# Kernel optimization log

Measured on AMD Instinct MI355X. Metric: run time of the kernel, lower is better.

## Reference

```python
import math
import jax, jax.numpy as jnp
import numpy as np

DIM = 4096
N_HEADS = 32
N_KV_HEADS = 8
HEAD_DIM = DIM // N_HEADS  # 128
N_REP = N_HEADS // N_KV_HEADS  # 4
BSZ = 1
SEQLEN = 2048
ROPE_THETA = 500000.0


def setup_inputs() -> dict:
    key = jax.random.key(0)
    ks = jax.random.split(key, 8)
    s = 1.0 / math.sqrt(DIM)
    x = jax.random.normal(ks[0], (BSZ, SEQLEN, DIM), dtype=jnp.float32)
    wq = jax.random.normal(ks[1], (DIM, N_HEADS * HEAD_DIM), dtype=jnp.float32) * s
    wk = jax.random.normal(ks[2], (DIM, N_KV_HEADS * HEAD_DIM), dtype=jnp.float32) * s
    wv = jax.random.normal(ks[3], (DIM, N_KV_HEADS * HEAD_DIM), dtype=jnp.float32) * s
    wo = jax.random.normal(ks[4], (N_HEADS * HEAD_DIM, DIM), dtype=jnp.float32) * s
    # RoPE frequencies: freqs_cis[t, j] = exp(i * t * theta^{-2j/hd})
    inv_freq = 1.0 / (ROPE_THETA ** (jnp.arange(0, HEAD_DIM, 2, dtype=jnp.float32) / HEAD_DIM))
    t = jnp.arange(SEQLEN, dtype=jnp.float32)
    angles = jnp.outer(t, inv_freq)  # [S, hd/2]
    freqs_cos = jnp.cos(angles)
    freqs_sin = jnp.sin(angles)
    # causal additive mask [S, S]: 0 on/below diagonal, -inf above
    mask = jnp.triu(jnp.full((SEQLEN, SEQLEN), float('-inf'), dtype=jnp.float32), k=1)
    cache_k = jnp.zeros((BSZ, SEQLEN, N_KV_HEADS, HEAD_DIM), dtype=jnp.float32)
    cache_v = jnp.zeros((BSZ, SEQLEN, N_KV_HEADS, HEAD_DIM), dtype=jnp.float32)
    return {"x": x, "wq": wq, "wk": wk, "wv": wv, "wo": wo,
            "freqs_cos": freqs_cos, "freqs_sin": freqs_sin, "mask": mask,
            "cache_k": cache_k, "cache_v": cache_v, "start_pos": 0}


def _apply_rotary(xq, xk, cos, sin):
    # xq: [B,S,Hq,hd], xk: [B,S,Hkv,hd]; cos/sin: [S, hd/2]
    def rot(x):
        b, s, h, d = x.shape
        xr = x.reshape(b, s, h, d // 2, 2)
        a, bb = xr[..., 0], xr[..., 1]
        c = cos[None, :, None, :]
        sn = sin[None, :, None, :]
        out = jnp.stack([a * c - bb * sn, a * sn + bb * c], axis=-1)
        return out.reshape(b, s, h, d)
    return rot(xq), rot(xk)


def reference(x, wq, wk, wv, wo, freqs_cos, freqs_sin, mask, cache_k, cache_v, start_pos):
    bsz, seqlen, _ = x.shape
    xq = (x @ wq).reshape(bsz, seqlen, N_HEADS, HEAD_DIM)
    xk = (x @ wk).reshape(bsz, seqlen, N_KV_HEADS, HEAD_DIM)
    xv = (x @ wv).reshape(bsz, seqlen, N_KV_HEADS, HEAD_DIM)
    xq, xk = _apply_rotary(xq, xk, freqs_cos, freqs_sin)
    # KV-cache append
    cache_k = jax.lax.dynamic_update_slice(cache_k, xk, (0, start_pos, 0, 0))
    cache_v = jax.lax.dynamic_update_slice(cache_v, xv, (0, start_pos, 0, 0))
    kv_len = start_pos + seqlen
    keys = cache_k[:, :kv_len]    # [B, T, Hkv, hd]
    values = cache_v[:, :kv_len]
    # GQA repeat (logical; einsum reshaping keeps math identical)
    keys = jnp.repeat(keys, N_REP, axis=2)      # [B, T, Hq, hd]
    values = jnp.repeat(values, N_REP, axis=2)
    scale = 1.0 / math.sqrt(HEAD_DIM)
    scores = jnp.einsum('bqhd,bkhd->bhqk', xq, keys) * scale
    scores = scores + mask[None, None, :, :kv_len]
    probs = jax.nn.softmax(scores.astype(jnp.float32), axis=-1).astype(xq.dtype)
    out = jnp.einsum('bhqk,bkhd->bqhd', probs, values)
    out = out.reshape(bsz, seqlen, N_HEADS * HEAD_DIM)
    return out @ wo
```

## Files before the change

### kernel.cpp

```cpp
#include <hip/hip_runtime.h>
#include <hip/hip_bf16.h>

typedef unsigned short u16;
typedef short short8 __attribute__((ext_vector_type(8)));
typedef float floatx4 __attribute__((ext_vector_type(4)));

#define DIM 4096
#define SEQ 2048
#define NH 32
#define NKV 8
#define HD 128
#define QKV_N 6144

static __device__ __forceinline__ float b2f(u16 u) {
    return __uint_as_float(((unsigned int)u) << 16);
}
static __device__ __forceinline__ u16 f2b(float f) {
    unsigned int u = __float_as_uint(f);
    u = (u + 0x7FFFu + ((u >> 16) & 1u)) >> 16;
    return (u16)u;
}
static __device__ __forceinline__ void async16(const u16* g, u16* l) {
    __builtin_amdgcn_global_load_lds((const __attribute__((address_space(1))) void*)g,
                                     (__attribute__((address_space(3))) void*)l, 16, 0, 0);
}

__global__ __launch_bounds__(256) void transpose_f32_bf16(const float* __restrict__ src,
                                                          u16* __restrict__ dst,
                                                          int R, int C) {
    __shared__ u16 tile[32][33];
    int c0 = blockIdx.x * 32, r0 = blockIdx.y * 32;
    int x = threadIdx.x & 31, y0 = threadIdx.x >> 5;
#pragma unroll
    for (int i = 0; i < 4; i++) {
        int r = y0 + i * 8;
        tile[r][x] = f2b(src[(size_t)(r0 + r) * C + c0 + x]);
    }
    __syncthreads();
#pragma unroll
    for (int i = 0; i < 4; i++) {
        int r = y0 + i * 8;
        dst[(size_t)(c0 + r) * R + r0 + x] = tile[x][r];
    }
}

__global__ __launch_bounds__(256) void convert_f32_bf16(const float* __restrict__ src,
                                                        u16* __restrict__ dst) {
    int i = (blockIdx.x * 256 + threadIdx.x) * 4;
    float4 f = *(const float4*)(src + i);
    ushort4 o;
    o.x = f2b(f.x); o.y = f2b(f.y); o.z = f2b(f.z); o.w = f2b(f.w);
    *(ushort4*)(dst + i) = o;
}

__global__ __launch_bounds__(256) void transpose_v(const u16* __restrict__ Xqkv,
                                                   u16* __restrict__ VT) {
    __shared__ u16 tile[32][33];
    int k0 = blockIdx.x * 32, d0 = blockIdx.y * 32, h = blockIdx.z;
    const u16* src = Xqkv + DIM + NKV * HD + h * HD;
    int x = threadIdx.x & 31, y0 = threadIdx.x >> 5;
#pragma unroll
    for (int i = 0; i < 4; i++) {
        int r = y0 + i * 8;
        tile[r][x] = src[(size_t)(k0 + r) * QKV_N + d0 + x];
    }
    __syncthreads();
    u16* dst = VT + ((size_t)h * HD + d0) * SEQ + k0;
#pragma unroll
    for (int i = 0; i < 4; i++) {
        int r = y0 + i * 8;
        dst[(size_t)r * SEQ + x] = tile[x][r];
    }
}

template<bool CF32>
__global__ __launch_bounds__(256) void gemm_bf16(const u16* __restrict__ A,
                                                 const u16* __restrict__ Bt,
                                                 void* __restrict__ Cv,
                                                 int M, int N, int K) {
    __shared__ u16 As[128 * 32];
    __shared__ u16 Bs[128 * 32];
    int tid = threadIdx.x;
    int wave = tid >> 6, lane = tid & 63, quad = lane >> 4, l16 = lane & 15;
    int wrow = (wave >> 1) * 64, wcol = (wave & 1) * 64;
    int m0 = blockIdx.y * 128, n0 = blockIdx.x * 128;

    int g = (lane & 3) ^ ((lane >> 3) & 3);
    int srow = lane >> 2;
    const u16* Ap = A + (size_t)(m0 + wave * 32 + srow) * K + g * 8;
    const u16* Bp = Bt + (size_t)(n0 + wave * 32 + srow) * K + g * 8;
    u16* As0 = &As[wave * 1024];
    u16* Bs0 = &Bs[wave * 1024];
    int sA = quad ^ ((l16 >> 1) & 3);

    floatx4 acc[4][4];
#pragma unroll
    for (int i = 0; i < 4; i++)
#pragma unroll
        for (int j = 0; j < 4; j++) acc[i][j] = (floatx4){0.f, 0.f, 0.f, 0.f};

    int nk = K >> 5;
    for (int kb = 0; kb < nk; kb++) {
        __syncthreads();
        const u16* a0 = Ap + kb * 32;
        const u16* b0 = Bp + kb * 32;
        async16(a0, As0);
        async16(a0 + (size_t)16 * K, As0 + 512);
        async16(b0, Bs0);
        async16(b0 + (size_t)16 * K, Bs0 + 512);
        __syncthreads();
        short8 a[4], b[4];
#pragma unroll
        for (int mt = 0; mt < 4; mt++)
            a[mt] = *(const short8*)&As[(wrow + mt * 16 + l16) * 32 + sA * 8];
#pragma unroll
        for (int nt = 0; nt < 4; nt++)
            b[nt] = *(const short8*)&Bs[(wcol + nt * 16 + l16) * 32 + sA * 8];
#pragma unroll
        for (int mt = 0; mt < 4; mt++)
#pragma unroll
            for (int nt = 0; nt < 4; nt++)
                acc[mt][nt] = __builtin_amdgcn_mfma_f32_16x16x32_bf16(a[mt], b[nt], acc[mt][nt], 0, 0, 0);
    }

#pragma unroll
    for (int mt = 0; mt < 4; mt++)
#pragma unroll
        for (int nt = 0; nt < 4; nt++) {
            int row = m0 + wrow + mt * 16 + quad * 4;
            int col = n0 + wcol + nt * 16 + l16;
#pragma unroll
            for (int r = 0; r < 4; r++) {
                if constexpr (CF32)
                    ((float*)Cv)[(size_t)(row + r) * N + col] = acc[mt][nt][r];
                else
                    ((u16*)Cv)[(size_t)(row + r) * N + col] = f2b(acc[mt][nt][r]);
            }
        }
}

__global__ __launch_bounds__(256) void rope_kernel(u16* __restrict__ X,
                                                   const float* __restrict__ fc,
                                                   const float* __restrict__ fs) {
    int idx = blockIdx.x * 256 + threadIdx.x;
    int i = idx & 63;
    int rem = idx >> 6;
    int h = rem % 40;
    int pos = rem / 40;
    int col = (h < 32) ? (h * 128 + 2 * i) : (4096 + (h - 32) * 128 + 2 * i);
    size_t off = (size_t)pos * QKV_N + col;
    unsigned int pr = *(unsigned int*)&X[off];
    float a = b2f((u16)(pr & 0xffffu));
    float b = b2f((u16)(pr >> 16));
    float c = fc[pos * 64 + i];
    float s = fs[pos * 64 + i];
    float na = a * c - b * s;
    float nb = a * s + b * c;
    unsigned int outw = ((unsigned int)f2b(nb) << 16) | (unsigned int)f2b(na);
    *(unsigned int*)&X[off] = outw;
}

__global__ __launch_bounds__(256) void attn_kernel(const u16* __restrict__ Xqkv,
                                                   const u16* __restrict__ VT,
                                                   u16* __restrict__ O) {
    __shared__ u16 Ks[64 * 128];
    __shared__ u16 Vt[128 * 64];
    __shared__ u16 Ps[4 * 1024];
    int head = blockIdx.y;
    int kvh = head >> 2;
    const u16* Xq = Xqkv + head * HD;
    const u16* Xk = Xqkv + DIM + kvh * HD;
    const u16* Vg = VT + (size_t)kvh * HD * SEQ;
    int tid = threadIdx.x, wave = tid >> 6, lane = tid & 63, quad = lane >> 4, l16 = lane & 15;

    size_t offKe = (size_t)quad * QKV_N + (size_t)((l16 ^ quad) * 8);
    size_t offKo = (size_t)quad * QKV_N + (size_t)((l16 ^ (quad + 4)) * 8);
    size_t offV  = (size_t)(lane >> 3) * SEQ + (size_t)((((lane & 7) ^ ((lane >> 3) & 7))) * 8);
    int sK[4];
#pragma unroll
    for (int ks = 0; ks < 4; ks++) sK[ks] = (ks * 4 + quad) ^ (l16 & 7);

    const float scale = 0.08838834764831845f;

    for (int pass = 0; pass < 2; pass++) {
        int qb = pass ? (31 - blockIdx.x) : blockIdx.x;
        int q0 = qb * 64;

        short8 aq[4];
        {
            const u16* qp = Xq + (size_t)(q0 + wave * 16 + l16) * QKV_N + quad * 8;
#pragma unroll
            for (int ks = 0; ks < 4; ks++) aq[ks] = *(const short8*)(qp + ks * 32);
        }
        float l_i[4] = {0.f, 0.f, 0.f, 0.f};
        floatx4 o_acc[8];
#pragma unroll
        for (int i = 0; i < 8; i++) o_acc[i] = (floatx4){0.f, 0.f, 0.f, 0.f};

        for (int kb = 0; kb <= qb; kb++) {
            __syncthreads();
#pragma unroll
            for (int c = 0; c < 4; c++) {
                int kc = wave * 4 + c;
                const u16* gp = Xk + (size_t)(kb * 64 + kc * 4) * QKV_N + ((kc & 1) ? offKo : offKe);
                async16(gp, &Ks[kc * 512]);
            }
#pragma unroll
            for (int c = 0; c < 4; c++) {
                int vc = wave * 4 + c;
                async16(Vg + (size_t)(vc * 8) * SEQ + (size_t)(kb * 64) + offV, &Vt[vc * 512]);
            }
            __syncthreads();

            floatx4 s[4];
#pragma unroll
            for (int nt = 0; nt < 4; nt++) s[nt] = (floatx4){0.f, 0.f, 0.f, 0.f};
#pragma unroll
            for (int ks = 0; ks < 4; ks++) {
#pragma unroll
                for (int nt = 0; nt < 4; nt++) {
                    short8 bk = *(const short8*)&Ks[(nt * 16 + l16) * 128 + sK[ks] * 8];
                    s[nt] = __builtin_amdgcn_mfma_f32_16x16x32_bf16(aq[ks], bk, s[nt], 0, 0, 0);
                }
            }

            bool diag = (kb == qb);
            int qrel = wave * 16 + quad * 4;
            float rowsum[4] = {0.f, 0.f, 0.f, 0.f};
#pragma unroll
            for (int nt = 0; nt < 4; nt++) {
                int kcol = nt * 16 + l16;
#pragma unroll
                for (int r = 0; r < 4; r++) {
                    float v = s[nt][r] * scale;
                    if (diag && kcol > qrel + r) v = -__builtin_inff();
                    float p = __expf(fminf(v, 60.f));
                    s[nt][r] = p;
                    rowsum[r] += p;
                }
            }
#pragma unroll
            for (int m = 1; m < 16; m <<= 1)
#pragma unroll
                for (int r = 0; r < 4; r++)
                    rowsum[r] += __shfl_xor(rowsum[r], m);
#pragma unroll
            for (int r = 0; r < 4; r++) l_i[r] += rowsum[r];

            u16* pw = &Ps[wave * 1024];
#pragma unroll
            for (int nt = 0; nt < 4; nt++) {
                int gbase = nt * 2 + (l16 >> 3);
#pragma unroll
                for (int r = 0; r < 4; r++) {
                    int row = quad * 4 + r;
                    int slot = gbase ^ (row & 7);
                    unsigned u = __float_as_uint(s[nt][r]);
                    pw[row * 64 + slot * 8 + (l16 & 7)] = (u16)((u + 0x8000u) >> 16);
                }
            }

#pragma unroll
            for (int ks = 0; ks < 2; ks++) {
                short8 ap = *(const short8*)&Ps[wave * 1024 + l16 * 64 + sK[ks] * 8];
#pragma unroll
                for (int nt = 0; nt < 8; nt++) {
                    short8 bv = *(const short8*)&Vt[(nt * 16 + l16) * 64 + sK[ks] * 8];
                    o_acc[nt] = __builtin_amdgcn_mfma_f32_16x16x32_bf16(ap, bv, o_acc[nt], 0, 0, 0);
                }
            }
        }

        float invl[4];
#pragma unroll
        for (int r = 0; r < 4; r++) invl[r] = 1.f / l_i[r];
#pragma unroll
        for (int nt = 0; nt < 8; nt++) {
            int row = q0 + wave * 16 + quad * 4;
            int col = head * HD + nt * 16 + l16;
#pragma unroll
            for (int r = 0; r < 4; r++)
                O[(size_t)(row + r) * DIM + col] = f2b(o_acc[nt][r] * invl[r]);
        }
    }
}

extern "C" void kernel_launch(void* const* d_in, const int* in_sizes, int n_in,
                              void* d_out, int out_size, void* d_ws, size_t ws_size,
                              hipStream_t stream) {
    const float* x  = (const float*)d_in[0];
    const float* wq = (const float*)d_in[1];
    const float* wk = (const float*)d_in[2];
    const float* wv = (const float*)d_in[3];
    const float* wo = (const float*)d_in[4];
    const float* fc = (const float*)d_in[5];
    const float* fs = (const float*)d_in[6];

    u16* WT   = (u16*)d_ws;
    u16* Xqkv = WT + (size_t)QKV_N * DIM;
    u16* Obuf = Xqkv + (size_t)SEQ * QKV_N;
    u16* xbf  = Obuf;
    u16* VT   = WT + (size_t)5120 * DIM;
    float* outp = (float*)d_out;

    transpose_f32_bf16<<<dim3(128, 128), 256, 0, stream>>>(wq, WT, 4096, 4096);
    transpose_f32_bf16<<<dim3(32, 128), 256, 0, stream>>>(wk, WT + (size_t)4096 * 4096, 4096, 1024);
    transpose_f32_bf16<<<dim3(32, 128), 256, 0, stream>>>(wv, WT + (size_t)5120 * 4096, 4096, 1024);

    convert_f32_bf16<<<(SEQ * DIM) / 1024, 256, 0, stream>>>(x, xbf);

    gemm_bf16<false><<<dim3(QKV_N / 128, SEQ / 128), 256, 0, stream>>>(xbf, WT, Xqkv, SEQ, QKV_N, DIM);

    rope_kernel<<<(SEQ * 40 * 64) / 256, 256, 0, stream>>>(Xqkv, fc, fs);

    transpose_v<<<dim3(SEQ / 32, HD / 32, NKV), 256, 0, stream>>>(Xqkv, VT);

    attn_kernel<<<dim3(16, NH), 256, 0, stream>>>(Xqkv, VT, Obuf);

    transpose_f32_bf16<<<dim3(128, 128), 256, 0, stream>>>(wo, WT, 4096, 4096);

    gemm_bf16<true><<<dim3(DIM / 128, SEQ / 128), 256, 0, stream>>>(Obuf, WT, outp, SEQ, DIM, DIM);
}
```

Before: 563.4 us.

## Double-buffer K tiles in attention and vectorize weight transpose with 64x64 tiles

The attention kernel now double-buffers K tiles in shared memory, prefetching the next K block while the current one is computed, and issues the V load early with an extra barrier before the PV MFMAs. Separately, the fp32-to-bf16 weight transpose switches to 64x64 tiles with float4 loads, swizzled LDS slots and 16-byte vector stores, to cut scalar global traffic. The trade is more LDS for attention (a second K buffer) and an added barrier per key block.

Measured after the change: 569.5 us. No clear change (+1.1%).

```diff
diff --git a/kernel.cpp b/kernel.cpp
--- a/kernel.cpp
+++ b/kernel.cpp
@@ -3,6 +3,7 @@
 
 typedef unsigned short u16;
 typedef short short8 __attribute__((ext_vector_type(8)));
+typedef unsigned short ushort8v __attribute__((ext_vector_type(8)));
 typedef float floatx4 __attribute__((ext_vector_type(4)));
 
 #define DIM 4096
@@ -28,19 +29,37 @@
 __global__ __launch_bounds__(256) void transpose_f32_bf16(const float* __restrict__ src,
                                                           u16* __restrict__ dst,
                                                           int R, int C) {
-    __shared__ u16 tile[32][33];
-    int c0 = blockIdx.x * 32, r0 = blockIdx.y * 32;
-    int x = threadIdx.x & 31, y0 = threadIdx.x >> 5;
-#pragma unroll
-    for (int i = 0; i < 4; i++) {
-        int r = y0 + i * 8;
-        tile[r][x] = f2b(src[(size_t)(r0 + r) * C + c0 + x]);
+    __shared__ __attribute__((aligned(16))) u16 t72[64 * 72];
+    int c0 = blockIdx.x * 64, r0 = blockIdx.y * 64;
+    int tid = threadIdx.x;
+
+    {
+        int r = tid & 63, w = tid >> 6;
+        const float* sp = src + (size_t)(r0 + r) * C + c0 + w * 16;
+        int m = r >> 3, rlo = r & 7;
+#pragma unroll
+        for (int j = 0; j < 4; j++) {
+            float4 f = *(const float4*)(sp + j * 4);
+            float fe[4] = {f.x, f.y, f.z, f.w};
+#pragma unroll
+            for (int e = 0; e < 4; e++) {
+                int c = w * 16 + j * 4 + e;
+                int slot = m ^ ((c & 3) << 1) ^ (c >> 3);
+                t72[c * 72 + slot * 8 + rlo] = f2b(fe[e]);
+            }
+        }
     }
     __syncthreads();
-#pragma unroll
-    for (int i = 0; i < 4; i++) {
-        int r = y0 + i * 8;
-        dst[(size_t)(c0 + r) * R + r0 + x] = tile[x][r];
+    {
+        int c = tid >> 2, mg = (tid & 3) * 2;
+        u16* dp = dst + (size_t)(c0 + c) * R + r0;
+#pragma unroll
+        for (int j = 0; j < 2; j++) {
+            int m = mg + j;
+            int slot = m ^ ((c & 3) << 1) ^ (c >> 3);
+            ushort8v v = *(const ushort8v*)&t72[c * 72 + slot * 8];
+            *(ushort8v*)(dp + m * 8) = v;
+        }
     }
 }
 
@@ -78,8 +97,8 @@
                                                  const u16* __restrict__ Bt,
                                                  void* __restrict__ Cv,
                                                  int M, int N, int K) {
-    __shared__ u16 As[128 * 32];
-    __shared__ u16 Bs[128 * 32];
+    __shared__ __attribute__((aligned(16))) u16 As[128 * 32];
+    __shared__ __attribute__((aligned(16))) u16 Bs[128 * 32];
     int tid = threadIdx.x;
     int wave = tid >> 6, lane = tid & 63, quad = lane >> 4, l16 = lane & 15;
     int wrow = (wave >> 1) * 64, wcol = (wave & 1) * 64;
@@ -163,9 +182,9 @@
 __global__ __launch_bounds__(256) void attn_kernel(const u16* __restrict__ Xqkv,
                                                    const u16* __restrict__ VT,
                                                    u16* __restrict__ O) {
-    __shared__ u16 Ks[64 * 128];
-    __shared__ u16 Vt[128 * 64];
-    __shared__ u16 Ps[4 * 1024];
+    __shared__ __attribute__((aligned(16))) u16 Ks[2 * 64 * 128];
+    __shared__ __attribute__((aligned(16))) u16 Vt[128 * 64];
+    __shared__ __attribute__((aligned(16))) u16 Ps[4 * 1024];
     int head = blockIdx.y;
     int kvh = head >> 2;
     const u16* Xq = Xqkv + head * HD;
@@ -197,21 +216,36 @@
 #pragma unroll
         for (int i = 0; i < 8; i++) o_acc[i] = (floatx4){0.f, 0.f, 0.f, 0.f};
 
-        for (int kb = 0; kb <= qb; kb++) {
-            __syncthreads();
+        if (pass) __syncthreads();
+        {
 #pragma unroll
             for (int c = 0; c < 4; c++) {
                 int kc = wave * 4 + c;
-                const u16* gp = Xk + (size_t)(kb * 64 + kc * 4) * QKV_N + ((kc & 1) ? offKo : offKe);
+                const u16* gp = Xk + (size_t)(kc * 4) * QKV_N + ((kc & 1) ? offKo : offKe);
                 async16(gp, &Ks[kc * 512]);
             }
-#pragma unroll
-            for (int c = 0; c < 4; c++) {
-                int vc = wave * 4 + c;
-                async16(Vg + (size_t)(vc * 8) * SEQ + (size_t)(kb * 64) + offV, &Vt[vc * 512]);
-            }
+        }
+
+        for (int kb = 0; kb <= qb; kb++) {
+            int cur = kb & 1;
             __syncthreads();
-
+            {
+#pragma unroll
+                for (int c = 0; c < 4; c++) {
+                    int vc = wave * 4 + c;
+                    async16(Vg + (size_t)(vc * 8) * SEQ + (size_t)(kb * 64) + offV, &Vt[vc * 512]);
+                }
+            }
+            if (kb < qb) {
+#pragma unroll
+                for (int c = 0; c < 4; c++) {
+                    int kc = wave * 4 + c;
+                    const u16* gp = Xk + (size_t)((kb + 1) * 64 + kc * 4) * QKV_N + ((kc & 1) ? offKo : offKe);
+                    async16(gp, &Ks[(cur ^ 1) * 8192 + kc * 512]);
+                }
+            }
+
+            const u16* kbase = &Ks[cur * 8192];
             floatx4 s[4];
 #pragma unroll
             for (int nt = 0; nt < 4; nt++) s[nt] = (floatx4){0.f, 0.f, 0.f, 0.f};
@@ -219,7 +253,7 @@
             for (int ks = 0; ks < 4; ks++) {
 #pragma unroll
                 for (int nt = 0; nt < 4; nt++) {
-                    short8 bk = *(const short8*)&Ks[(nt * 16 + l16) * 128 + sK[ks] * 8];
+                    short8 bk = *(const short8*)&kbase[(nt * 16 + l16) * 128 + sK[ks] * 8];
                     s[nt] = __builtin_amdgcn_mfma_f32_16x16x32_bf16(aq[ks], bk, s[nt], 0, 0, 0);
                 }
             }
@@ -259,6 +293,8 @@
                     pw[row * 64 + slot * 8 + (l16 & 7)] = (u16)((u + 0x8000u) >> 16);
                 }
             }
+
+            __syncthreads();
 
 #pragma unroll
             for (int ks = 0; ks < 2; ks++) {
@@ -303,9 +339,9 @@
     u16* VT   = WT + (size_t)5120 * DIM;
     float* outp = (float*)d_out;
 
-    transpose_f32_bf16<<<dim3(128, 128), 256, 0, stream>>>(wq, WT, 4096, 4096);
-    transpose_f32_bf16<<<dim3(32, 128), 256, 0, stream>>>(wk, WT + (size_t)4096 * 4096, 4096, 1024);
-    transpose_f32_bf16<<<dim3(32, 128), 256, 0, stream>>>(wv, WT + (size_t)5120 * 4096, 4096, 1024);
+    transpose_f32_bf16<<<dim3(64, 64), 256, 0, stream>>>(wq, WT, 4096, 4096);
+    transpose_f32_bf16<<<dim3(16, 64), 256, 0, stream>>>(wk, WT + (size_t)4096 * 4096, 4096, 1024);
+    transpose_f32_bf16<<<dim3(16, 64), 256, 0, stream>>>(wv, WT + (size_t)5120 * 4096, 4096, 1024);
 
     convert_f32_bf16<<<(SEQ * DIM) / 1024, 256, 0, stream>>>(x, xbf);
 
@@ -317,7 +353,7 @@
 
     attn_kernel<<<dim3(16, NH), 256, 0, stream>>>(Xqkv, VT, Obuf);
 
-    transpose_f32_bf16<<<dim3(128, 128), 256, 0, stream>>>(wo, WT, 4096, 4096);
+    transpose_f32_bf16<<<dim3(64, 64), 256, 0, stream>>>(wo, WT, 4096, 4096);
 
     gemm_bf16<true><<<dim3(DIM / 128, SEQ / 128), 256, 0, stream>>>(Obuf, WT, outp, SEQ, DIM, DIM);
 }
```
